# Performance work log

Hardware: AMD Instinct MI355X
Metric: run time of the kernel (lower is better)

Reference implementation:

```python
import jax, jax.numpy as jnp
import numpy as np

B, H, W, DIM, R = 8, 64, 64, 768, 16
_DN = ('NHWC', 'HWIO', 'NHWC')


def _conv(x, k):
    # stride-1 SAME conv == torch Conv2d(padding=k//2) for 3x3 and 1x1 kernels
    return jax.lax.conv_general_dilated(x, k, (1, 1), 'SAME', dimension_numbers=_DN)


def setup_inputs() -> dict:
    key = jax.random.key(0)
    ks = jax.random.split(key, 16)
    s = 0.02
    return {
        'x': jax.random.normal(ks[0], (B, H, W, DIM), jnp.float32),
        'W_qkv': jax.random.normal(ks[1], (DIM, 3 * DIM), jnp.float32) * s,
        'b_qkv': jax.random.normal(ks[2], (3 * DIM,), jnp.float32) * s,
        'Wa_q': jax.random.normal(ks[3], (DIM, R), jnp.float32) * s,
        'Wb_q': jax.random.normal(ks[4], (R, DIM), jnp.float32) * s,
        'Wa_v': jax.random.normal(ks[5], (DIM, R), jnp.float32) * s,
        'Wb_v': jax.random.normal(ks[6], (R, DIM), jnp.float32) * s,
        'K_q3': jax.random.normal(ks[7], (3, 3, R, R), jnp.float32) * s,
        'b_q3': jax.random.normal(ks[8], (R,), jnp.float32) * s,
        'K_v3': jax.random.normal(ks[9], (3, 3, R, R), jnp.float32) * s,
        'b_v3': jax.random.normal(ks[10], (R,), jnp.float32) * s,
        'K_q1': jax.random.normal(ks[11], (1, 1, R, R), jnp.float32) * s,
        'b_q1': jax.random.normal(ks[12], (R,), jnp.float32) * s,
        'K_v1': jax.random.normal(ks[13], (1, 1, R, R), jnp.float32) * s,
        'b_v1': jax.random.normal(ks[14], (R,), jnp.float32) * s,
    }


def reference(x, W_qkv, b_qkv, Wa_q, Wb_q, Wa_v, Wb_v,
              K_q3, b_q3, K_v3, b_v3, K_q1, b_q1, K_v1, b_v1):
    dim = x.shape[-1]
    # base QKV projection: [B,H,W,3*dim]
    qkv = jnp.einsum('bhwc,cd->bhwd', x, W_qkv) + b_qkv
    # low-rank down-projections: [B,H,W,r]
    a_q = x @ Wa_q
    a_v = x @ Wa_v
    # NHWC convs replace the permute->conv->permute dance in the torch code
    mid_q = _conv(a_q, K_q3) + b_q3 + _conv(a_q, K_q1) + b_q1 + a_q
    mid_v = _conv(a_v, K_v3) + b_v3 + _conv(a_v, K_v1) + b_v1 + a_v
    new_q = mid_q @ Wb_q  # [B,H,W,dim]
    new_v = mid_v @ Wb_v
    qkv = qkv.at[..., :dim].add(new_q)
    qkv = qkv.at[..., -dim:].add(new_v)
    return qkv
```

## Files before the change

kernel.cpp:

```cpp
#include <hip/hip_runtime.h>

typedef __bf16 bf16;
typedef __attribute__((ext_vector_type(8))) __bf16 bf16x8;
typedef __attribute__((ext_vector_type(4))) float f32x4;

#define AS1U(p) ((const __attribute__((address_space(1))) unsigned int*)(p))
#define AS3U(p) ((__attribute__((address_space(3))) unsigned int*)(p))

__device__ __forceinline__ unsigned short f2bf(float f) {
    union { float f; unsigned int u; } a; a.f = f;
    unsigned int u = a.u;
    u += 0x7fffu + ((u >> 16) & 1u);
    return (unsigned short)(u >> 16);
}

#define MTOT 32768
#define DIM  768
#define KP   832
#define NOUT 2304

__global__ __launch_bounds__(256) void bbuild_kernel(
    const float* __restrict__ Wqkv, const float* __restrict__ Wbq,
    const float* __restrict__ Wbv, unsigned short* __restrict__ Bt)
{
    int idx = blockIdx.x * 256 + threadIdx.x;
    int k = idx % KP;
    int n = idx / KP;
    float v = 0.f;
    if (k < 768) {
        v = Wqkv[(size_t)k * NOUT + n];
    } else if (k < 784) {
        if (n < 768) v = Wbq[(size_t)(k - 768) * 768 + n];
    } else if (k < 800) {
        if (n >= 1536) v = Wbv[(size_t)(k - 784) * 768 + (n - 1536)];
    }
    Bt[idx] = f2bf(v);
}

__global__ __launch_bounds__(256) void prep_kernel(
    const float* __restrict__ x, const float* __restrict__ Waq,
    const float* __restrict__ Wav, unsigned short* __restrict__ Ap,
    float* __restrict__ aq, float* __restrict__ av)
{
    __shared__ float Xs[64][65];
    __shared__ float Was[64][32];
    const int t = threadIdx.x;
    const int p0 = blockIdx.x * 64;
    const int pix = t & 63;
    const int j0 = (t >> 6) * 8;
    float acc[8] = {0.f,0.f,0.f,0.f,0.f,0.f,0.f,0.f};

    for (int kt = 0; kt < 12; ++kt) {
        __syncthreads();
        #pragma unroll
        for (int it = 0; it < 4; ++it) {
            int idx = it * 256 + t;
            int pp = idx >> 4;
            int c4 = (idx & 15) * 4;
            const float4 v = *(const float4*)(x + (size_t)(p0 + pp) * DIM + kt * 64 + c4);
            ushort4 u; u.x = f2bf(v.x); u.y = f2bf(v.y); u.z = f2bf(v.z); u.w = f2bf(v.w);
            *(ushort4*)(Ap + (size_t)(p0 + pp) * KP + kt * 64 + c4) = u;
            Xs[pp][c4 + 0] = v.x; Xs[pp][c4 + 1] = v.y;
            Xs[pp][c4 + 2] = v.z; Xs[pp][c4 + 3] = v.w;
        }
        {
            int r = t >> 2;
            int cc = (t & 3) * 8;
            #pragma unroll
            for (int j = 0; j < 8; ++j) {
                int col = cc + j;
                float wv = (col < 16) ? Waq[(size_t)(kt * 64 + r) * 16 + col]
                                      : Wav[(size_t)(kt * 64 + r) * 16 + (col - 16)];
                Was[r][col] = wv;
            }
        }
        __syncthreads();
        for (int c = 0; c < 64; ++c) {
            float xv = Xs[pix][c];
            float4 w0 = *(const float4*)&Was[c][j0];
            float4 w1 = *(const float4*)&Was[c][j0 + 4];
            acc[0] += xv * w0.x; acc[1] += xv * w0.y; acc[2] += xv * w0.z; acc[3] += xv * w0.w;
            acc[4] += xv * w1.x; acc[5] += xv * w1.y; acc[6] += xv * w1.z; acc[7] += xv * w1.w;
        }
    }
    float* dst = (j0 < 16) ? (aq + (size_t)(p0 + pix) * 16 + j0)
                           : (av + (size_t)(p0 + pix) * 16 + (j0 - 16));
    #pragma unroll
    for (int j = 0; j < 8; ++j) dst[j] = acc[j];
    {
        int pp = t >> 2, cc = (t & 3) * 8;
        ushort4 z; z.x = 0; z.y = 0; z.z = 0; z.w = 0;
        *(ushort4*)(Ap + (size_t)(p0 + pp) * KP + 800 + cc) = z;
        *(ushort4*)(Ap + (size_t)(p0 + pp) * KP + 804 + cc) = z;
    }
}

__global__ __launch_bounds__(256) void conv_mid_kernel(
    const float* __restrict__ aq, const float* __restrict__ av,
    const float* __restrict__ Kq3, const float* __restrict__ bq3,
    const float* __restrict__ Kv3, const float* __restrict__ bv3,
    const float* __restrict__ Kq1, const float* __restrict__ bq1,
    const float* __restrict__ Kv1, const float* __restrict__ bv1,
    unsigned short* __restrict__ Ap)
{
    const int bx = blockIdx.x;
    const int qv   = bx & 1;
    const int tile = (bx >> 1) & 15;
    const int b    = bx >> 5;
    const float* a  = qv ? av  : aq;
    const float* K3 = qv ? Kv3 : Kq3;
    const float* K1 = qv ? Kv1 : Kq1;
    const float* b3 = qv ? bv3 : bq3;
    const float* b1 = qv ? bv1 : bq1;

    __shared__ float K3s[9][16][16];
    __shared__ float K1s[16][16];
    const int t = threadIdx.x;
    for (int i = t; i < 9 * 256; i += 256) ((float*)K3s)[i] = K3[i];
    ((float*)K1s)[t] = K1[t];
    __syncthreads();

    const int lh = t >> 4, lw = t & 15;
    const int h = (tile >> 2) * 16 + lh;
    const int w = (tile & 3) * 16 + lw;

    float acc[16];
    const float* ac = a + (((size_t)b * 64 + h) * 64 + w) * 16;
    float cen[16];
    #pragma unroll
    for (int i4 = 0; i4 < 4; ++i4) {
        float4 q = ((const float4*)ac)[i4];
        cen[i4 * 4 + 0] = q.x; cen[i4 * 4 + 1] = q.y;
        cen[i4 * 4 + 2] = q.z; cen[i4 * 4 + 3] = q.w;
    }
    #pragma unroll
    for (int o = 0; o < 16; ++o) acc[o] = b3[o] + b1[o] + cen[o];
    #pragma unroll
    for (int i = 0; i < 16; ++i) {
        float vi = cen[i];
        #pragma unroll
        for (int o = 0; o < 16; ++o) acc[o] += vi * K1s[i][o];
    }
    for (int dh = -1; dh <= 1; ++dh) {
        for (int dw = -1; dw <= 1; ++dw) {
            int hh = h + dh, ww = w + dw;
            if ((unsigned)hh < 64u && (unsigned)ww < 64u) {
                const float* ap = a + (((size_t)b * 64 + hh) * 64 + ww) * 16;
                float v[16];
                #pragma unroll
                for (int i4 = 0; i4 < 4; ++i4) {
                    float4 q = ((const float4*)ap)[i4];
                    v[i4 * 4 + 0] = q.x; v[i4 * 4 + 1] = q.y;
                    v[i4 * 4 + 2] = q.z; v[i4 * 4 + 3] = q.w;
                }
                const int tap = (dh + 1) * 3 + (dw + 1);
                #pragma unroll
                for (int i = 0; i < 16; ++i) {
                    float vi = v[i];
                    #pragma unroll
                    for (int o = 0; o < 16; ++o) acc[o] += vi * K3s[tap][i][o];
                }
            }
        }
    }
    unsigned short* dst = Ap + (((size_t)b * 64 + h) * 64 + w) * KP + 768 + qv * 16;
    #pragma unroll
    for (int o4 = 0; o4 < 4; ++o4) {
        ushort4 u;
        u.x = f2bf(acc[o4 * 4 + 0]); u.y = f2bf(acc[o4 * 4 + 1]);
        u.z = f2bf(acc[o4 * 4 + 2]); u.w = f2bf(acc[o4 * 4 + 3]);
        *(ushort4*)(dst + o4 * 4) = u;
    }
}

__global__ __launch_bounds__(256, 2) void gemm_kernel(
    const bf16* __restrict__ A, const bf16* __restrict__ Bt,
    const float* __restrict__ bias, float* __restrict__ out)
{
    __shared__ bf16 As[128 * 64];
    __shared__ bf16 Bs[128 * 64];
    const int t = threadIdx.x;
    const int wave = t >> 6, lane = t & 63;
    const int m0 = blockIdx.y * 128, n0 = blockIdx.x * 128;
    const int wm = wave & 1, wn = wave >> 1;

    f32x4 acc[4][4] = {};

    const int sr = lane >> 3;
    const int ql = (lane & 7) ^ sr;

    for (int kt = 0; kt < 13; ++kt) {
        const int k0 = kt * 64;
        __syncthreads();
        #pragma unroll
        for (int it = 0; it < 4; ++it) {
            int ci = wave * 4 + it;
            int r = ci * 8 + sr;
            const bf16* ga = A  + (size_t)(m0 + r) * KP + k0 + ql * 8;
            __builtin_amdgcn_global_load_lds(AS1U(ga), AS3U(As + ci * 512 + lane * 8), 16, 0, 0);
            const bf16* gb = Bt + (size_t)(n0 + r) * KP + k0 + ql * 8;
            __builtin_amdgcn_global_load_lds(AS1U(gb), AS3U(Bs + ci * 512 + lane * 8), 16, 0, 0);
        }
        __syncthreads();
        #pragma unroll
        for (int kk = 0; kk < 2; ++kk) {
            bf16x8 af[4], bfr[4];
            const int phys = ((kk << 2) + (lane >> 4)) ^ (lane & 7);
            #pragma unroll
            for (int mi = 0; mi < 4; ++mi) {
                int rr = wm * 64 + mi * 16 + (lane & 15);
                af[mi] = *(const bf16x8*)(As + rr * 64 + phys * 8);
            }
            #pragma unroll
            for (int ni = 0; ni < 4; ++ni) {
                int rr = wn * 64 + ni * 16 + (lane & 15);
                bfr[ni] = *(const bf16x8*)(Bs + rr * 64 + phys * 8);
            }
            #pragma unroll
            for (int mi = 0; mi < 4; ++mi)
                #pragma unroll
                for (int ni = 0; ni < 4; ++ni)
                    acc[mi][ni] = __builtin_amdgcn_mfma_f32_16x16x32_bf16(
                        af[mi], bfr[ni], acc[mi][ni], 0, 0, 0);
        }
    }
    #pragma unroll
    for (int ni = 0; ni < 4; ++ni) {
        int col = n0 + wn * 64 + ni * 16 + (lane & 15);
        float bv = bias[col];
        #pragma unroll
        for (int mi = 0; mi < 4; ++mi) {
            int rbase = m0 + wm * 64 + mi * 16 + ((lane >> 4) << 2);
            #pragma unroll
            for (int r = 0; r < 4; ++r)
                out[(size_t)(rbase + r) * NOUT + col] = acc[mi][ni][r] + bv;
        }
    }
}

extern "C" void kernel_launch(void* const* d_in, const int* in_sizes, int n_in,
                              void* d_out, int out_size, void* d_ws, size_t ws_size,
                              hipStream_t stream) {
    const float* x    = (const float*)d_in[0];
    const float* Wqkv = (const float*)d_in[1];
    const float* bqkv = (const float*)d_in[2];
    const float* Waq  = (const float*)d_in[3];
    const float* Wbq  = (const float*)d_in[4];
    const float* Wav  = (const float*)d_in[5];
    const float* Wbv  = (const float*)d_in[6];
    const float* Kq3  = (const float*)d_in[7];
    const float* bq3  = (const float*)d_in[8];
    const float* Kv3  = (const float*)d_in[9];
    const float* bv3  = (const float*)d_in[10];
    const float* Kq1  = (const float*)d_in[11];
    const float* bq1  = (const float*)d_in[12];
    const float* Kv1  = (const float*)d_in[13];
    const float* bv1  = (const float*)d_in[14];
    float* out = (float*)d_out;

    char* ws = (char*)d_ws;
    unsigned short* Ap = (unsigned short*)ws;
    float* aq = (float*)(ws + 54525952);
    float* av = (float*)(ws + 54525952 + 2097152);
    unsigned short* Bt = (unsigned short*)(ws + 54525952 + 4194304);

    bbuild_kernel<<<(NOUT * KP) / 256, 256, 0, stream>>>(Wqkv, Wbq, Wbv, Bt);
    prep_kernel<<<MTOT / 64, 256, 0, stream>>>(x, Waq, Wav, Ap, aq, av);
    conv_mid_kernel<<<256, 256, 0, stream>>>(aq, av, Kq3, bq3, Kv3, bv3,
                                             Kq1, bq1, Kv1, bv1, Ap);
    gemm_kernel<<<dim3(NOUT / 128, MTOT / 128), 256, 0, stream>>>(
        (const bf16*)Ap, (const bf16*)Bt, bqkv, out);
}
```

Baseline: 603.9 us.

## Use MFMA for low-rank down-projection and tile the weight transpose

```diff
diff --git a/kernel.cpp b/kernel.cpp
--- a/kernel.cpp
+++ b/kernel.cpp
@@ -13,6 +13,9 @@
     u += 0x7fffu + ((u >> 16) & 1u);
     return (unsigned short)(u >> 16);
 }
+__device__ __forceinline__ unsigned int pk2(float a, float b) {
+    return (unsigned int)f2bf(a) | ((unsigned int)f2bf(b) << 16);
+}
 
 #define MTOT 32768
 #define DIM  768
@@ -21,78 +24,112 @@
 
 __global__ __launch_bounds__(256) void bbuild_kernel(
     const float* __restrict__ Wqkv, const float* __restrict__ Wbq,
-    const float* __restrict__ Wbv, unsigned short* __restrict__ Bt)
+    const float* __restrict__ Wbv, const float* __restrict__ Waq,
+    const float* __restrict__ Wav, unsigned short* __restrict__ Bt,
+    unsigned short* __restrict__ WaT)
 {
-    int idx = blockIdx.x * 256 + threadIdx.x;
-    int k = idx % KP;
-    int n = idx / KP;
-    float v = 0.f;
-    if (k < 768) {
-        v = Wqkv[(size_t)k * NOUT + n];
-    } else if (k < 784) {
-        if (n < 768) v = Wbq[(size_t)(k - 768) * 768 + n];
-    } else if (k < 800) {
-        if (n >= 1536) v = Wbv[(size_t)(k - 784) * 768 + (n - 1536)];
-    }
-    Bt[idx] = f2bf(v);
-}
-
-__global__ __launch_bounds__(256) void prep_kernel(
-    const float* __restrict__ x, const float* __restrict__ Waq,
-    const float* __restrict__ Wav, unsigned short* __restrict__ Ap,
-    float* __restrict__ aq, float* __restrict__ av)
-{
-    __shared__ float Xs[64][65];
-    __shared__ float Was[64][32];
+    const int bx = blockIdx.x;
     const int t = threadIdx.x;
-    const int p0 = blockIdx.x * 64;
-    const int pix = t & 63;
-    const int j0 = (t >> 6) * 8;
-    float acc[8] = {0.f,0.f,0.f,0.f,0.f,0.f,0.f,0.f};
-
-    for (int kt = 0; kt < 12; ++kt) {
-        __syncthreads();
+    if (bx < 432) {
+        __shared__ float Ts[64][65];
+        const int kt = bx % 12, nt = bx / 12;
         #pragma unroll
         for (int it = 0; it < 4; ++it) {
             int idx = it * 256 + t;
-            int pp = idx >> 4;
-            int c4 = (idx & 15) * 4;
-            const float4 v = *(const float4*)(x + (size_t)(p0 + pp) * DIM + kt * 64 + c4);
-            ushort4 u; u.x = f2bf(v.x); u.y = f2bf(v.y); u.z = f2bf(v.z); u.w = f2bf(v.w);
-            *(ushort4*)(Ap + (size_t)(p0 + pp) * KP + kt * 64 + c4) = u;
-            Xs[pp][c4 + 0] = v.x; Xs[pp][c4 + 1] = v.y;
-            Xs[pp][c4 + 2] = v.z; Xs[pp][c4 + 3] = v.w;
-        }
-        {
-            int r = t >> 2;
-            int cc = (t & 3) * 8;
-            #pragma unroll
-            for (int j = 0; j < 8; ++j) {
-                int col = cc + j;
-                float wv = (col < 16) ? Waq[(size_t)(kt * 64 + r) * 16 + col]
-                                      : Wav[(size_t)(kt * 64 + r) * 16 + (col - 16)];
-                Was[r][col] = wv;
-            }
-        }
-        __syncthreads();
-        for (int c = 0; c < 64; ++c) {
-            float xv = Xs[pix][c];
-            float4 w0 = *(const float4*)&Was[c][j0];
-            float4 w1 = *(const float4*)&Was[c][j0 + 4];
-            acc[0] += xv * w0.x; acc[1] += xv * w0.y; acc[2] += xv * w0.z; acc[3] += xv * w0.w;
-            acc[4] += xv * w1.x; acc[5] += xv * w1.y; acc[6] += xv * w1.z; acc[7] += xv * w1.w;
-        }
-    }
-    float* dst = (j0 < 16) ? (aq + (size_t)(p0 + pix) * 16 + j0)
-                           : (av + (size_t)(p0 + pix) * 16 + (j0 - 16));
-    #pragma unroll
-    for (int j = 0; j < 8; ++j) dst[j] = acc[j];
-    {
-        int pp = t >> 2, cc = (t & 3) * 8;
-        ushort4 z; z.x = 0; z.y = 0; z.z = 0; z.w = 0;
-        *(ushort4*)(Ap + (size_t)(p0 + pp) * KP + 800 + cc) = z;
-        *(ushort4*)(Ap + (size_t)(p0 + pp) * KP + 804 + cc) = z;
-    }
+            int kr = idx >> 4;
+            int nc = (idx & 15) * 4;
+            float4 v = *(const float4*)(Wqkv + (size_t)(kt * 64 + kr) * NOUT + nt * 64 + nc);
+            Ts[kr][nc + 0] = v.x; Ts[kr][nc + 1] = v.y;
+            Ts[kr][nc + 2] = v.z; Ts[kr][nc + 3] = v.w;
+        }
+        __syncthreads();
+        #pragma unroll
+        for (int it = 0; it < 4; ++it) {
+            int idx = it * 256 + t;
+            int nr = idx >> 4;
+            int kc = (idx & 15) * 4;
+            ushort4 u;
+            u.x = f2bf(Ts[kc + 0][nr]); u.y = f2bf(Ts[kc + 1][nr]);
+            u.z = f2bf(Ts[kc + 2][nr]); u.w = f2bf(Ts[kc + 3][nr]);
+            *(ushort4*)(Bt + (size_t)(nt * 64 + nr) * KP + kt * 64 + kc) = u;
+        }
+    } else if (bx < 576) {
+        int idx = (bx - 432) * 256 + t;
+        int n = idx >> 4;
+        int k = 768 + (idx & 15) * 4;
+        ushort4 u;
+        unsigned short* up = (unsigned short*)&u;
+        #pragma unroll
+        for (int j = 0; j < 4; ++j) {
+            int kk = k + j;
+            float v = 0.f;
+            if (kk < 784) { if (n < 768) v = Wbq[(size_t)(kk - 768) * 768 + n]; }
+            else if (kk < 800) { if (n >= 1536) v = Wbv[(size_t)(kk - 784) * 768 + (n - 1536)]; }
+            up[j] = f2bf(v);
+        }
+        *(ushort4*)(Bt + (size_t)n * KP + k) = u;
+    } else {
+        int idx = (bx - 576) * 256 + t;
+        int n = idx / 768, k = idx % 768;
+        float v = (n < 16) ? Waq[(size_t)k * 16 + n] : Wav[(size_t)k * 16 + (n - 16)];
+        WaT[(size_t)n * 768 + k] = f2bf(v);
+    }
+}
+
+__global__ __launch_bounds__(256) void prep_kernel(
+    const float* __restrict__ x, const bf16* __restrict__ WaT,
+    unsigned short* __restrict__ Ap, float* __restrict__ aq, float* __restrict__ av)
+{
+    __shared__ bf16 Xs[64 * 64];
+    const int t = threadIdx.x;
+    const int wave = t >> 6, lane = t & 63;
+    const int l15 = lane & 15, q = lane >> 4;
+    const int p0 = blockIdx.x * 64;
+    const int row = t >> 2, c16 = (t & 3) * 16;
+    const int r8 = row & 7, ch0 = c16 >> 3;
+    f32x4 acc[2] = {};
+
+    for (int kt = 0; kt < 12; ++kt) {
+        const float* xp = x + (size_t)(p0 + row) * DIM + kt * 64 + c16;
+        float4 v0 = *(const float4*)(xp + 0);
+        float4 v1 = *(const float4*)(xp + 4);
+        float4 v2 = *(const float4*)(xp + 8);
+        float4 v3 = *(const float4*)(xp + 12);
+        uint4 u0, u1;
+        u0.x = pk2(v0.x, v0.y); u0.y = pk2(v0.z, v0.w);
+        u0.z = pk2(v1.x, v1.y); u0.w = pk2(v1.z, v1.w);
+        u1.x = pk2(v2.x, v2.y); u1.y = pk2(v2.z, v2.w);
+        u1.z = pk2(v3.x, v3.y); u1.w = pk2(v3.z, v3.w);
+        unsigned short* apq = Ap + (size_t)(p0 + row) * KP + kt * 64 + c16;
+        *(uint4*)(apq) = u0;
+        *(uint4*)(apq + 8) = u1;
+        __syncthreads();
+        *(uint4*)(Xs + row * 64 + ((ch0 + 0) ^ r8) * 8) = u0;
+        *(uint4*)(Xs + row * 64 + ((ch0 + 1) ^ r8) * 8) = u1;
+        __syncthreads();
+        bf16x8 bfr[2][2];
+        #pragma unroll
+        for (int kk = 0; kk < 2; ++kk)
+            #pragma unroll
+            for (int nf = 0; nf < 2; ++nf)
+                bfr[kk][nf] = *(const bf16x8*)(WaT + (size_t)(nf * 16 + l15) * 768
+                                               + kt * 64 + kk * 32 + q * 8);
+        #pragma unroll
+        for (int kk = 0; kk < 2; ++kk) {
+            int phys = ((kk << 2) + q) ^ (l15 & 7);
+            bf16x8 af = *(const bf16x8*)(Xs + (wave * 16 + l15) * 64 + phys * 8);
+            acc[0] = __builtin_amdgcn_mfma_f32_16x16x32_bf16(af, bfr[kk][0], acc[0], 0, 0, 0);
+            acc[1] = __builtin_amdgcn_mfma_f32_16x16x32_bf16(af, bfr[kk][1], acc[1], 0, 0, 0);
+        }
+    }
+    const int m = wave * 16 + q * 4;
+    #pragma unroll
+    for (int r = 0; r < 4; ++r) {
+        aq[(size_t)(p0 + m + r) * 16 + l15] = acc[0][r];
+        av[(size_t)(p0 + m + r) * 16 + l15] = acc[1][r];
+    }
+    uint4 z; z.x = z.y = z.z = z.w = 0u;
+    *(uint4*)(Ap + (size_t)(p0 + row) * KP + 800 + (t & 3) * 8) = z;
 }
 
 __global__ __launch_bounds__(256) void conv_mid_kernel(
@@ -129,9 +166,9 @@
     float cen[16];
     #pragma unroll
     for (int i4 = 0; i4 < 4; ++i4) {
-        float4 q = ((const float4*)ac)[i4];
-        cen[i4 * 4 + 0] = q.x; cen[i4 * 4 + 1] = q.y;
-        cen[i4 * 4 + 2] = q.z; cen[i4 * 4 + 3] = q.w;
+        float4 qd = ((const float4*)ac)[i4];
+        cen[i4 * 4 + 0] = qd.x; cen[i4 * 4 + 1] = qd.y;
+        cen[i4 * 4 + 2] = qd.z; cen[i4 * 4 + 3] = qd.w;
     }
     #pragma unroll
     for (int o = 0; o < 16; ++o) acc[o] = b3[o] + b1[o] + cen[o];
@@ -149,9 +186,9 @@
                 float v[16];
                 #pragma unroll
                 for (int i4 = 0; i4 < 4; ++i4) {
-                    float4 q = ((const float4*)ap)[i4];
-                    v[i4 * 4 + 0] = q.x; v[i4 * 4 + 1] = q.y;
-                    v[i4 * 4 + 2] = q.z; v[i4 * 4 + 3] = q.w;
+                    float4 qd = ((const float4*)ap)[i4];
+                    v[i4 * 4 + 0] = qd.x; v[i4 * 4 + 1] = qd.y;
+                    v[i4 * 4 + 2] = qd.z; v[i4 * 4 + 3] = qd.w;
                 }
                 const int tap = (dh + 1) * 3 + (dw + 1);
                 #pragma unroll
@@ -259,13 +296,14 @@
     float* out = (float*)d_out;
 
     char* ws = (char*)d_ws;
-    unsigned short* Ap = (unsigned short*)ws;
-    float* aq = (float*)(ws + 54525952);
-    float* av = (float*)(ws + 54525952 + 2097152);
-    unsigned short* Bt = (unsigned short*)(ws + 54525952 + 4194304);
-
-    bbuild_kernel<<<(NOUT * KP) / 256, 256, 0, stream>>>(Wqkv, Wbq, Wbv, Bt);
-    prep_kernel<<<MTOT / 64, 256, 0, stream>>>(x, Waq, Wav, Ap, aq, av);
+    unsigned short* Ap  = (unsigned short*)ws;
+    float* aq           = (float*)(ws + 54525952);
+    float* av           = (float*)(ws + 54525952 + 2097152);
+    unsigned short* Bt  = (unsigned short*)(ws + 54525952 + 4194304);
+    unsigned short* WaT = (unsigned short*)(ws + 62554112);
+
+    bbuild_kernel<<<672, 256, 0, stream>>>(Wqkv, Wbq, Wbv, Waq, Wav, Bt, WaT);
+    prep_kernel<<<MTOT / 64, 256, 0, stream>>>(x, (const bf16*)WaT, Ap, aq, av);
     conv_mid_kernel<<<256, 256, 0, stream>>>(aq, av, Kq3, bq3, Kv3, bv3,
                                              Kq1, bq1, Kv1, bv1, Ap);
     gemm_kernel<<<dim3(NOUT / 128, MTOT / 128), 256, 0, stream>>>(
```

Result: faster. 553.3 us (-8.4%).
